# Kernel optimization log

Measured on AMD Instinct MI355X. Metric: run time of the kernel, lower is better.

## Reference

```python
import jax, jax.numpy as jnp
import numpy as np

D_MODEL = 768
D_STATE = 16
D_CONV = 4
EXPAND = 2
INNER = EXPAND * D_MODEL  # 1536
BATCH = 2
SEQLEN = 2048


def setup_inputs() -> dict:
    key = jax.random.key(0)
    ks = jax.random.split(key, 8)
    s = 0.02
    return {
        "hidden_states": jax.random.normal(ks[0], (BATCH, SEQLEN, D_MODEL), jnp.float32),
        "in_proj_w": jax.random.normal(ks[1], (2 * INNER, D_MODEL), jnp.float32) * (D_MODEL ** -0.5),
        "out_proj_w": jax.random.normal(ks[2], (D_MODEL, INNER), jnp.float32) * (INNER ** -0.5),
        "dt_proj_w": jax.random.normal(ks[3], (INNER, INNER), jnp.float32) * (INNER ** -0.5),
        "dt_proj_b": jnp.zeros((INNER,), jnp.float32),
        "conv_w": jax.random.normal(ks[4], (INNER, D_CONV), jnp.float32) * s,
        "conv_b": jnp.zeros((INNER,), jnp.float32),
        "A_log": jnp.zeros((INNER, D_STATE), jnp.float32),
        "B_param": jax.random.normal(ks[5], (INNER, D_STATE), jnp.float32) * s,
        "C_param": jax.random.normal(ks[6], (INNER, D_STATE), jnp.float32) * s,
        "D_param": jnp.ones((INNER,), jnp.float32),
        "dt_bias": jnp.zeros((INNER,), jnp.float32),
    }


def reference(hidden_states, in_proj_w, out_proj_w, dt_proj_w, dt_proj_b,
              conv_w, conv_b, A_log, B_param, C_param, D_param, dt_bias):
    # in_proj: (B, L, d_model) -> (B, L, 2*inner); split into projected / gate
    xz = jnp.einsum('bld,od->blo', hidden_states, in_proj_w)
    proj, gate = jnp.split(xz, 2, axis=-1)
    x = jnp.transpose(proj, (0, 2, 1))  # (B, inner, L) channel-first

    # depthwise causal conv (left-pad d_conv-1) + bias + SiLU
    conv = jax.lax.conv_general_dilated(
        x, conv_w[:, None, :], window_strides=(1,),
        padding=[(D_CONV - 1, 0)], feature_group_count=INNER,
        dimension_numbers=('NCH', 'OIH', 'NCH'))
    u = jax.nn.silu(conv + conv_b[None, :, None])  # (B, inner, L)

    # dt projection (1x1 linear on channel-first) + softplus(dt + dt_bias)
    delta = jnp.einsum('oc,bcl->bol', dt_proj_w, u) + dt_proj_b[None, :, None]
    dt = jax.nn.softplus(delta + dt_bias[None, :, None])  # (B, inner, L)

    A = -jnp.exp(A_log)  # (inner, d_state)
    # discretize: dA = exp(dt * A), dBu = dt * u * B   -> (B, inner, L, N)
    dA = jnp.exp(dt[..., None] * A[None, :, None, :])
    dBu = (dt * u)[..., None] * B_param[None, :, None, :]

    dA_t = jnp.moveaxis(dA, 2, 0)    # (L, B, inner, N)
    dBu_t = jnp.moveaxis(dBu, 2, 0)  # (L, B, inner, N)

    def step(h, inp):
        a_t, b_t = inp
        h = a_t * h + b_t                      # (B, inner, N)
        y = jnp.einsum('bdn,dn->bd', h, C_param)
        return h, y

    h0 = jnp.zeros(dA_t.shape[1:], dA.dtype)
    _, ys = jax.lax.scan(step, h0, (dA_t, dBu_t))  # ys: (L, B, inner)
    y = jnp.transpose(ys, (1, 2, 0))               # (B, inner, L)

    z = jnp.transpose(gate, (0, 2, 1))             # (B, inner, L)
    y = (y + D_param[None, :, None] * u) * jax.nn.silu(z)

    # out_proj: (B, inner, L) -> (B, L, d_model)
    return jnp.einsum('bdl,od->blo', y, out_proj_w)
```

## Files before the change

kernel.cpp:

```cpp
#include <hip/hip_runtime.h>
#include <cstdint>
#include <cstddef>

#define D_MODEL 768
#define D_STATE 16
#define D_CONV  4
#define INNER   1536
#define BATCH   2
#define SEQLEN  2048
#define M_TOK   (BATCH * SEQLEN)
#define NCH     (BATCH * INNER)
#define NCHUNK  64
#define CL      (SEQLEN / NCHUNK)

typedef unsigned short u16;
typedef __attribute__((ext_vector_type(4))) unsigned short us4;
typedef __attribute__((ext_vector_type(8))) short bf8;
typedef __attribute__((ext_vector_type(4))) float f32x4;
typedef __attribute__((ext_vector_type(4))) int i32x4;

#define INV254 (1.f / 254.f)

__device__ __forceinline__ u16 f2bf(float f) {
    uint32_t x = __float_as_uint(f);
    return (u16)((x + 0x7fffu + ((x >> 16) & 1u)) >> 16);
}
__device__ __forceinline__ float bf2f(u16 h) {
    return __uint_as_float(((uint32_t)h) << 16);
}
__device__ __forceinline__ int pk8(float a, float b, float c, float d) {
    return ((int)a & 0xff) | (((int)b & 0xff) << 8) |
           (((int)c & 0xff) << 16) | (((int)d & 0xff) << 24);
}

__global__ __launch_bounds__(256) void rowquant(
    const float* __restrict__ src, int8_t* __restrict__ q1,
    int8_t* __restrict__ q0, float* __restrict__ sc, int K)
{
    const int row = blockIdx.x;
    const float* r = src + (size_t)row * K;
    const int tid = threadIdx.x;

    float mx = 0.f;
    for (int i = tid * 4; i < K; i += 1024) {
        const float4 v = *(const float4*)(r + i);
        mx = fmaxf(mx, fmaxf(fmaxf(fabsf(v.x), fabsf(v.y)),
                             fmaxf(fabsf(v.z), fabsf(v.w))));
    }
#pragma unroll
    for (int off = 1; off < 64; off <<= 1)
        mx = fmaxf(mx, __shfl_xor(mx, off, 64));
    __shared__ float red[4];
    if ((tid & 63) == 0) red[tid >> 6] = mx;
    __syncthreads();
    const float rm = fmaxf(fmaxf(red[0], red[1]), fmaxf(red[2], red[3]));
    const float q = rm > 0.f ? 127.f / rm : 0.f;

    for (int i = tid * 4; i < K; i += 1024) {
        const float4 v = *(const float4*)(r + i);
        float s1[4], s0[4];
        const float xv[4] = {v.x, v.y, v.z, v.w};
#pragma unroll
        for (int e = 0; e < 4; ++e) {
            const float t = xv[e] * q;
            s1[e] = rintf(t);
            s0[e] = rintf((t - s1[e]) * 254.f);
        }
        const size_t o = ((size_t)row * K + i) >> 2;
        ((int*)q1)[o] = pk8(s1[0], s1[1], s1[2], s1[3]);
        ((int*)q0)[o] = pk8(s0[0], s0[1], s0[2], s0[3]);
    }
    if (tid == 0) sc[row] = rm * (1.f / 127.f);
}

__global__ __launch_bounds__(256) void cvt_hilo(
    const float* __restrict__ x, u16* __restrict__ hi, u16* __restrict__ lo, int n4)
{
    const int i = blockIdx.x * 256 + threadIdx.x;
    if (i >= n4) return;
    const float4 v = ((const float4*)x)[i];
    us4 h, l;
    h.x = f2bf(v.x); l.x = f2bf(v.x - bf2f(h.x));
    h.y = f2bf(v.y); l.y = f2bf(v.y - bf2f(h.y));
    h.z = f2bf(v.z); l.z = f2bf(v.z - bf2f(h.z));
    h.w = f2bf(v.w); l.w = f2bf(v.w - bf2f(h.w));
    ((us4*)hi)[i] = h;
    ((us4*)lo)[i] = l;
}

template <int MODE, int FRM, int FRN>
__global__ __launch_bounds__(256) void gemm_i8(
    const int8_t* __restrict__ A1g, const int8_t* __restrict__ A0g,
    const int8_t* __restrict__ B1g, const int8_t* __restrict__ B0g,
    const float* __restrict__ scA, const float* __restrict__ scB,
    float* __restrict__ C, const float* __restrict__ bias1,
    const float* __restrict__ bias2, int M, int N, int K)
{
    constexpr int BM = FRM * 32;
    constexpr int BN = FRN * 32;
    constexpr int SBUF = (BM + BN) * 128;
    __shared__ __align__(16) char smem[2 * SBUF];

    const int tid = threadIdx.x;
    const int w = tid >> 6;
    const int lane = tid & 63;

    const int gx = gridDim.x;
    const int nwg = gx * gridDim.y;
    int f = blockIdx.y * gx + blockIdx.x;
    f = (f & 7) * (nwg >> 3) + (f >> 3);
    const int bm = (f / gx) * BM;
    const int bn = (f % gx) * BN;

    const int wm = (w >> 1) * (FRM * 16);
    const int wn = (w & 1) * (FRN * 16);

    const int g8 = lane & 7;
    const int r8 = lane >> 3;
    const int srcg = g8 ^ r8;
    const int sbyte = (srcg & 3) * 16;
    const bool use_lo = (srcg & 4) != 0;

    const int8_t* pA[FRM];
    const int8_t* pB[FRN];
#pragma unroll
    for (int c = 0; c < FRM; ++c) {
        const int row = w * (FRM * 8) + c * 8 + r8;
        pA[c] = (use_lo ? A0g : A1g) + (size_t)(bm + row) * K + sbyte;
    }
#pragma unroll
    for (int c = 0; c < FRN; ++c) {
        const int row = w * (FRN * 8) + c * 8 + r8;
        pB[c] = (use_lo ? B0g : B1g) + (size_t)(bn + row) * K + sbyte;
    }

    i32x4 acc1[FRM][FRN] = {};
    i32x4 acc2[FRM][FRN] = {};
    const int fr = lane & 15;
    const int gk = lane >> 4;
    const int ghi = gk ^ (fr & 7);

    const int aoff1 = (wm + fr) * 128 + ghi * 16;
    const int aoff0 = (wm + fr) * 128 + (ghi ^ 4) * 16;
    const int boff1 = BM * 128 + (wn + fr) * 128 + ghi * 16;
    const int boff0 = BM * 128 + (wn + fr) * 128 + (ghi ^ 4) * 16;
    const char* const S0 = smem;
    const char* const S1 = smem + SBUF;

    const int nt = K >> 6;

#define STAGE_ALL(sb, kt)                                                           \
    {                                                                               \
        _Pragma("unroll")                                                           \
        for (int c = 0; c < FRM; ++c)                                               \
            __builtin_amdgcn_global_load_lds(                                       \
                (const __attribute__((address_space(1))) void*)(pA[c] + (kt)),      \
                (__attribute__((address_space(3))) void*)((char*)(sb) + (w * FRM + c) * 1024), \
                16, 0, 0);                                                          \
        _Pragma("unroll")                                                           \
        for (int c = 0; c < FRN; ++c)                                               \
            __builtin_amdgcn_global_load_lds(                                       \
                (const __attribute__((address_space(1))) void*)(pB[c] + (kt)),      \
                (__attribute__((address_space(3))) void*)((char*)(sb) + BM * 128 + (w * FRN + c) * 1024), \
                16, 0, 0);                                                          \
    }

#define WAIT_COUNTED()                                                              \
    if constexpr (FRM + FRN == 8) { asm volatile("s_waitcnt vmcnt(8)" ::: "memory"); } \
    else if constexpr (FRM + FRN == 6) { asm volatile("s_waitcnt vmcnt(6)" ::: "memory"); } \
    else { asm volatile("s_waitcnt vmcnt(4)" ::: "memory"); }

#define COMPUTE(S)                                                                  \
    {                                                                               \
        i32x4 a1[FRM], a0[FRM], b1[FRN], b0[FRN];                                   \
        _Pragma("unroll")                                                           \
        for (int i = 0; i < FRM; ++i) {                                             \
            a1[i] = *(const i32x4*)((S) + aoff1 + i * 2048);                        \
            a0[i] = *(const i32x4*)((S) + aoff0 + i * 2048);                        \
        }                                                                           \
        _Pragma("unroll")                                                           \
        for (int j = 0; j < FRN; ++j) {                                             \
            b1[j] = *(const i32x4*)((S) + boff1 + j * 2048);                        \
            b0[j] = *(const i32x4*)((S) + boff0 + j * 2048);                        \
        }                                                                           \
        _Pragma("unroll")                                                           \
        for (int i = 0; i < FRM; ++i)                                               \
            _Pragma("unroll")                                                       \
            for (int j = 0; j < FRN; ++j) {                                         \
                acc1[i][j] = __builtin_amdgcn_mfma_i32_16x16x64_i8(a1[i], b1[j], acc1[i][j], 0, 0, 0); \
                acc2[i][j] = __builtin_amdgcn_mfma_i32_16x16x64_i8(a1[i], b0[j], acc2[i][j], 0, 0, 0); \
                acc2[i][j] = __builtin_amdgcn_mfma_i32_16x16x64_i8(a0[i], b1[j], acc2[i][j], 0, 0, 0); \
            }                                                                       \
    }

    STAGE_ALL(S0, 0)

    for (int t = 0; t < nt; t += 2) {
        STAGE_ALL(S1, (t + 1) * 64)
        WAIT_COUNTED()
        __builtin_amdgcn_s_barrier();
        __builtin_amdgcn_sched_barrier(0);
        __builtin_amdgcn_s_setprio(1);
        COMPUTE(S0)
        __builtin_amdgcn_s_setprio(0);
        __builtin_amdgcn_sched_barrier(0);
        __builtin_amdgcn_s_barrier();

        const int k2 = (t + 2 < nt) ? (t + 2) * 64 : (nt - 1) * 64;
        STAGE_ALL(S0, k2)
        WAIT_COUNTED()
        __builtin_amdgcn_s_barrier();
        __builtin_amdgcn_sched_barrier(0);
        __builtin_amdgcn_s_setprio(1);
        COMPUTE(S1)
        __builtin_amdgcn_s_setprio(0);
        __builtin_amdgcn_sched_barrier(0);
        __builtin_amdgcn_s_barrier();
    }
#undef STAGE_ALL
#undef WAIT_COUNTED
#undef COMPUTE

    const int r0 = (lane >> 4) * 4;
#pragma unroll
    for (int i = 0; i < FRM; ++i) {
        const int row0 = bm + wm + i * 16 + r0;
        float sA[4];
#pragma unroll
        for (int r = 0; r < 4; ++r) sA[r] = scA[row0 + r];
#pragma unroll
        for (int j = 0; j < FRN; ++j) {
            const int col = bn + wn + j * 16 + fr;
            const float sB = scB[col];
            float add = 0.f;
            if constexpr (MODE == 1) add = bias1[col] + bias2[col];
#pragma unroll
            for (int r = 0; r < 4; ++r) {
                float v = ((float)acc1[i][j][r] +
                           (float)acc2[i][j][r] * INV254) * (sA[r] * sB);
                if constexpr (MODE == 1) {
                    const float xx = v + add;
                    v = (xx > 20.f) ? xx : log1pf(expf(xx));
                }
                C[(size_t)(row0 + r) * N + col] = v;
            }
        }
    }
}

template <int MODE, int FRM, int FRN>
__global__ __launch_bounds__(256) void gemm_mfma(
    const u16* __restrict__ Ah_g, const u16* __restrict__ Al_g,
    const u16* __restrict__ Bh_g, const u16* __restrict__ Bl_g,
    float* __restrict__ C, const float* __restrict__ bias1,
    const float* __restrict__ bias2, int M, int N, int K)
{
    constexpr int BM = FRM * 32;
    constexpr int BN = FRN * 32;
    constexpr int SBUF = (BM + BN) * 128;
    __shared__ __align__(16) char smem[2 * SBUF];

    const int tid = threadIdx.x;
    const int w = tid >> 6;
    const int lane = tid & 63;

    const int gx = gridDim.x;
    const int nwg = gx * gridDim.y;
    int f = blockIdx.y * gx + blockIdx.x;
    f = (f & 7) * (nwg >> 3) + (f >> 3);
    const int bm = (f / gx) * BM;
    const int bn = (f % gx) * BN;

    const int wm = (w >> 1) * (FRM * 16);
    const int wn = (w & 1) * (FRN * 16);

    const int g8 = lane & 7;
    const int r8 = lane >> 3;
    const int srcg = g8 ^ r8;
    const int scol = (srcg & 3) * 8;
    const bool use_lo = (srcg & 4) != 0;

    const u16* pA[FRM];
    const u16* pB[FRN];
#pragma unroll
    for (int c = 0; c < FRM; ++c) {
        const int row = w * (FRM * 8) + c * 8 + r8;
        pA[c] = (use_lo ? Al_g : Ah_g) + (size_t)(bm + row) * K + scol;
    }
#pragma unroll
    for (int c = 0; c < FRN; ++c) {
        const int row = w * (FRN * 8) + c * 8 + r8;
        pB[c] = (use_lo ? Bl_g : Bh_g) + (size_t)(bn + row) * K + scol;
    }

    f32x4 acc[FRM][FRN] = {};
    const int fr = lane & 15;
    const int gk = lane >> 4;
    const int ghi = gk ^ (fr & 7);

    const int aoff_h = (wm + fr) * 128 + ghi * 16;
    const int aoff_l = (wm + fr) * 128 + (ghi ^ 4) * 16;
    const int boff_h = BM * 128 + (wn + fr) * 128 + ghi * 16;
    const int boff_l = BM * 128 + (wn + fr) * 128 + (ghi ^ 4) * 16;
    const char* const S0 = smem;
    const char* const S1 = smem + SBUF;

    const int nt = K >> 5;

#define STAGE_ALL(sb, kt)                                                           \
    {                                                                               \
        _Pragma("unroll")                                                           \
        for (int c = 0; c < FRM; ++c)                                               \
            __builtin_amdgcn_global_load_lds(                                       \
                (const __attribute__((address_space(1))) void*)(pA[c] + (kt)),      \
                (__attribute__((address_space(3))) void*)((char*)(sb) + (w * FRM + c) * 1024), \
                16, 0, 0);                                                          \
        _Pragma("unroll")                                                           \
        for (int c = 0; c < FRN; ++c)                                               \
            __builtin_amdgcn_global_load_lds(                                       \
                (const __attribute__((address_space(1))) void*)(pB[c] + (kt)),      \
                (__attribute__((address_space(3))) void*)((char*)(sb) + BM * 128 + (w * FRN + c) * 1024), \
                16, 0, 0);                                                          \
    }

#define WAIT_COUNTED()                                                              \
    if constexpr (FRM + FRN == 8) { asm volatile("s_waitcnt vmcnt(8)" ::: "memory"); } \
    else if constexpr (FRM + FRN == 6) { asm volatile("s_waitcnt vmcnt(6)" ::: "memory"); } \
    else { asm volatile("s_waitcnt vmcnt(4)" ::: "memory"); }

#define COMPUTE(S)                                                                  \
    {                                                                               \
        bf8 ah[FRM], al[FRM], bh[FRN], bl[FRN];                                     \
        _Pragma("unroll")                                                           \
        for (int i = 0; i < FRM; ++i) {                                             \
            ah[i] = *(const bf8*)((S) + aoff_h + i * 2048);                         \
            al[i] = *(const bf8*)((S) + aoff_l + i * 2048);                         \
        }                                                                           \
        _Pragma("unroll")                                                           \
        for (int j = 0; j < FRN; ++j) {                                             \
            bh[j] = *(const bf8*)((S) + boff_h + j * 2048);                         \
            bl[j] = *(const bf8*)((S) + boff_l + j * 2048);                         \
        }                                                                           \
        _Pragma("unroll")                                                           \
        for (int i = 0; i < FRM; ++i)                                               \
            _Pragma("unroll")                                                       \
            for (int j = 0; j < FRN; ++j) {                                         \
                acc[i][j] = __builtin_amdgcn_mfma_f32_16x16x32_bf16(ah[i], bh[j], acc[i][j], 0, 0, 0); \
                acc[i][j] = __builtin_amdgcn_mfma_f32_16x16x32_bf16(ah[i], bl[j], acc[i][j], 0, 0, 0); \
                acc[i][j] = __builtin_amdgcn_mfma_f32_16x16x32_bf16(al[i], bh[j], acc[i][j], 0, 0, 0); \
            }                                                                       \
    }

    STAGE_ALL(S0, 0)

    for (int t = 0; t < nt; t += 2) {
        STAGE_ALL(S1, (t + 1) * 32)
        WAIT_COUNTED()
        __builtin_amdgcn_s_barrier();
        __builtin_amdgcn_sched_barrier(0);
        __builtin_amdgcn_s_setprio(1);
        COMPUTE(S0)
        __builtin_amdgcn_s_setprio(0);
        __builtin_amdgcn_sched_barrier(0);
        __builtin_amdgcn_s_barrier();

        const int k2 = (t + 2 < nt) ? (t + 2) * 32 : (nt - 1) * 32;
        STAGE_ALL(S0, k2)
        WAIT_COUNTED()
        __builtin_amdgcn_s_barrier();
        __builtin_amdgcn_sched_barrier(0);
        __builtin_amdgcn_s_setprio(1);
        COMPUTE(S1)
        __builtin_amdgcn_s_setprio(0);
        __builtin_amdgcn_sched_barrier(0);
        __builtin_amdgcn_s_barrier();
    }
#undef STAGE_ALL
#undef WAIT_COUNTED
#undef COMPUTE

    const int r0 = (lane >> 4) * 4;
#pragma unroll
    for (int i = 0; i < FRM; ++i) {
        const int row0 = bm + wm + i * 16 + r0;
#pragma unroll
        for (int j = 0; j < FRN; ++j) {
            const int col = bn + wn + j * 16 + fr;
            float add = 0.f;
            if constexpr (MODE == 1) add = bias1[col] + bias2[col];
#pragma unroll
            for (int r = 0; r < 4; ++r) {
                float v = acc[i][j][r];
                if constexpr (MODE == 1) {
                    const float xx = v + add;
                    v = (xx > 20.f) ? xx : log1pf(expf(xx));
                }
                C[(size_t)(row0 + r) * N + col] = v;
            }
        }
    }
}

__global__ __launch_bounds__(384) void conv_silu_quant(
    const float* __restrict__ xz, const float* __restrict__ cw,
    const float* __restrict__ cb, int8_t* __restrict__ u1,
    int8_t* __restrict__ u0, float* __restrict__ su)
{
    const int m = blockIdx.x;
    const int tid = threadIdx.x;
    const int c4 = tid * 4;
    const int b = m >> 11;
    const int l = m & (SEQLEN - 1);

    float wt[4][4];
#pragma unroll
    for (int i = 0; i < 4; ++i) {
        const float4 wv = *(const float4*)&cw[(c4 + i) * 4];
        wt[i][0] = wv.x; wt[i][1] = wv.y; wt[i][2] = wv.z; wt[i][3] = wv.w;
    }
    const float4 bias = *(const float4*)&cb[c4];
    float a[4] = {bias.x, bias.y, bias.z, bias.w};

#pragma unroll
    for (int j = 0; j < 4; ++j) {
        const int ll = l - 3 + j;
        if (ll >= 0) {
            const float4 x = *(const float4*)&xz[(size_t)(b * SEQLEN + ll) * (2 * INNER) + c4];
            a[0] = fmaf(x.x, wt[0][j], a[0]);
            a[1] = fmaf(x.y, wt[1][j], a[1]);
            a[2] = fmaf(x.z, wt[2][j], a[2]);
            a[3] = fmaf(x.w, wt[3][j], a[3]);
        }
    }
    float o[4];
#pragma unroll
    for (int i = 0; i < 4; ++i) o[i] = a[i] / (1.f + __expf(-a[i]));

    float mx = fmaxf(fmaxf(fabsf(o[0]), fabsf(o[1])),
                     fmaxf(fabsf(o[2]), fabsf(o[3])));
#pragma unroll
    for (int off = 1; off < 64; off <<= 1)
        mx = fmaxf(mx, __shfl_xor(mx, off, 64));
    __shared__ float red[6];
    if ((tid & 63) == 0) red[tid >> 6] = mx;
    __syncthreads();
    float rm = red[0];
#pragma unroll
    for (int i = 1; i < 6; ++i) rm = fmaxf(rm, red[i]);
    const float q = rm > 0.f ? 127.f / rm : 0.f;

    float s1[4], s0[4];
#pragma unroll
    for (int e = 0; e < 4; ++e) {
        const float t = o[e] * q;
        s1[e] = rintf(t);
        s0[e] = rintf((t - s1[e]) * 254.f);
    }
    const size_t vi = ((size_t)m * INNER + c4) >> 2;
    ((int*)u1)[vi] = pk8(s1[0], s1[1], s1[2], s1[3]);
    ((int*)u0)[vi] = pk8(s0[0], s0[1], s0[2], s0[3]);
    if (tid == 0) su[m] = rm * (1.f / 127.f);
}

__global__ __launch_bounds__(256) void scan_pass1(
    const float* __restrict__ dt, const int8_t* __restrict__ u1,
    const int8_t* __restrict__ u0, const float* __restrict__ su,
    const float* __restrict__ A_log, const float* __restrict__ Bp,
    float* __restrict__ hend, float* __restrict__ Sdt)
{
    const int ch = blockIdx.x * 256 + threadIdx.x;
    const int c = blockIdx.y;
    const int b = (ch >= INNER) ? 1 : 0;
    const int d = ch - b * INNER;

    float A2[D_STATE], Bn[D_STATE];
#pragma unroll
    for (int n = 0; n < D_STATE; n += 4) {
        const float4 av = *(const float4*)&A_log[d * D_STATE + n];
        const float4 bv = *(const float4*)&Bp[d * D_STATE + n];
        A2[n+0] = -expf(av.x) * 1.44269504f; Bn[n+0] = bv.x;
        A2[n+1] = -expf(av.y) * 1.44269504f; Bn[n+1] = bv.y;
        A2[n+2] = -expf(av.z) * 1.44269504f; Bn[n+2] = bv.z;
        A2[n+3] = -expf(av.w) * 1.44269504f; Bn[n+3] = bv.w;
    }

    const size_t base = (size_t)(b * SEQLEN + c * CL) * INNER + d;
    const float* dtp = dt + base;
    const int8_t* u1p = u1 + base;
    const int8_t* u0p = u0 + base;
    const float* sup = su + (b * SEQLEN + c * CL);

    float h[D_STATE] = {};
    float S = 0.f;

    float dtv = dtp[0];
    float uv = fmaf((float)u0p[0], INV254, (float)u1p[0]) * sup[0];

    for (int l = 0; l < CL; ++l) {
        float dtn = 0.f, un = 0.f;
        if (l + 1 < CL) {
            dtn = dtp[(size_t)(l + 1) * INNER];
            un = fmaf((float)u0p[(size_t)(l + 1) * INNER], INV254,
                      (float)u1p[(size_t)(l + 1) * INNER]) * sup[l + 1];
        }
        const float dtu = dtv * uv;
        S += dtv;
#pragma unroll
        for (int n = 0; n < D_STATE; ++n) {
            const float dA = exp2f(dtv * A2[n]);
            h[n] = fmaf(dA, h[n], dtu * Bn[n]);
        }
        dtv = dtn; uv = un;
    }

#pragma unroll
    for (int n = 0; n < D_STATE; ++n)
        hend[((size_t)c * D_STATE + n) * NCH + ch] = h[n];
    Sdt[(size_t)c * NCH + ch] = S;
}

__global__ __launch_bounds__(256) void scan_combine(
    const float* __restrict__ hend, const float* __restrict__ Sdt,
    const float* __restrict__ A_log, float* __restrict__ h0all)
{
    const int idx = blockIdx.x * 256 + threadIdx.x;
    const int n = idx / NCH;
    const int ch = idx - n * NCH;
    const int b = (ch >= INNER) ? 1 : 0;
    const int d = ch - b * INNER;
    const float A2 = -expf(A_log[d * D_STATE + n]) * 1.44269504f;

    float h0 = 0.f;
    for (int c = 0; c < NCHUNK; ++c) {
        const size_t o = ((size_t)c * D_STATE + n) * NCH + ch;
        h0all[o] = h0;
        const float P = exp2f(A2 * Sdt[(size_t)c * NCH + ch]);
        h0 = fmaf(P, h0, hend[o]);
    }
}

__global__ __launch_bounds__(256) void scan_pass2(
    const float* __restrict__ dt, const int8_t* __restrict__ u1,
    const int8_t* __restrict__ u0, const float* __restrict__ su,
    const float* __restrict__ xz, const float* __restrict__ A_log,
    const float* __restrict__ Bp, const float* __restrict__ Cp,
    const float* __restrict__ Dp, const float* __restrict__ h0all,
    u16* __restrict__ ygh, u16* __restrict__ ygl)
{
    const int ch = blockIdx.x * 256 + threadIdx.x;
    const int c = blockIdx.y;
    const int b = (ch >= INNER) ? 1 : 0;
    const int d = ch - b * INNER;

    float A2[D_STATE], Bn[D_STATE], Cn[D_STATE];
#pragma unroll
    for (int n = 0; n < D_STATE; n += 4) {
        const float4 av = *(const float4*)&A_log[d * D_STATE + n];
        const float4 bv = *(const float4*)&Bp[d * D_STATE + n];
        const float4 cv = *(const float4*)&Cp[d * D_STATE + n];
        A2[n+0] = -expf(av.x) * 1.44269504f; Bn[n+0] = bv.x; Cn[n+0] = cv.x;
        A2[n+1] = -expf(av.y) * 1.44269504f; Bn[n+1] = bv.y; Cn[n+1] = cv.y;
        A2[n+2] = -expf(av.z) * 1.44269504f; Bn[n+2] = bv.z; Cn[n+2] = cv.z;
        A2[n+3] = -expf(av.w) * 1.44269504f; Bn[n+3] = bv.w; Cn[n+3] = cv.w;
    }
    const float Dd = Dp[d];

    float h[D_STATE];
#pragma unroll
    for (int n = 0; n < D_STATE; ++n)
        h[n] = h0all[((size_t)c * D_STATE + n) * NCH + ch];

    const size_t base = (size_t)(b * SEQLEN + c * CL) * INNER + d;
    const float* dtp = dt + base;
    const int8_t* u1p = u1 + base;
    const int8_t* u0p = u0 + base;
    const float* sup = su + (b * SEQLEN + c * CL);
    const float* zp = xz + (size_t)(b * SEQLEN + c * CL) * (2 * INNER) + INNER + d;
    u16* yhp = ygh + base;
    u16* ylp = ygl + base;

    float dtv = dtp[0];
    float uv = fmaf((float)u0p[0], INV254, (float)u1p[0]) * sup[0];
    float zv = zp[0];

    for (int l = 0; l < CL; ++l) {
        float dtn = 0.f, un = 0.f, zn = 0.f;
        if (l + 1 < CL) {
            dtn = dtp[(size_t)(l + 1) * INNER];
            un = fmaf((float)u0p[(size_t)(l + 1) * INNER], INV254,
                      (float)u1p[(size_t)(l + 1) * INNER]) * sup[l + 1];
            zn = zp[(size_t)(l + 1) * (2 * INNER)];
        }
        const float dtu = dtv * uv;
        float y = 0.f;
#pragma unroll
        for (int n = 0; n < D_STATE; ++n) {
            const float dA = exp2f(dtv * A2[n]);
            h[n] = fmaf(dA, h[n], dtu * Bn[n]);
            y = fmaf(h[n], Cn[n], y);
        }
        const float sig = 1.f / (1.f + __expf(-zv));
        const float val = (y + Dd * uv) * (zv * sig);
        const u16 hv = f2bf(val);
        yhp[(size_t)l * INNER] = hv;
        ylp[(size_t)l * INNER] = f2bf(val - bf2f(hv));
        dtv = dtn; uv = un; zv = zn;
    }
}

extern "C" void kernel_launch(void* const* d_in, const int* in_sizes, int n_in,
                              void* d_out, int out_size, void* d_ws, size_t ws_size,
                              hipStream_t stream)
{
    const float* hs      = (const float*)d_in[0];
    const float* in_w    = (const float*)d_in[1];
    const float* out_w   = (const float*)d_in[2];
    const float* dt_w    = (const float*)d_in[3];
    const float* dt_b    = (const float*)d_in[4];
    const float* conv_w  = (const float*)d_in[5];
    const float* conv_b  = (const float*)d_in[6];
    const float* A_log   = (const float*)d_in[7];
    const float* Bp      = (const float*)d_in[8];
    const float* Cp      = (const float*)d_in[9];
    const float* Dp      = (const float*)d_in[10];
    const float* dt_bias = (const float*)d_in[11];
    float* out = (float*)d_out;

    float* xz    = (float*)d_ws;
    float* dtf   = xz + (size_t)M_TOK * 2 * INNER;
    float* hend  = dtf + (size_t)M_TOK * INNER;
    float* Sdt   = hend + (size_t)NCHUNK * D_STATE * NCH;
    float* h0all = Sdt + (size_t)NCHUNK * NCH;
    float* su_u  = h0all + (size_t)NCHUNK * D_STATE * NCH;
    float* sc_hs = su_u + M_TOK;
    float* sc_iw = sc_hs + M_TOK;
    float* sc_dw = sc_iw + 2 * INNER;
    u16* ygh = (u16*)(sc_dw + INNER);
    u16* ygl = ygh + (size_t)M_TOK * INNER;
    u16* owh = ygl + (size_t)M_TOK * INNER;
    u16* owl = owh + (size_t)D_MODEL * INNER;
    int8_t* hs1 = (int8_t*)(owl + (size_t)D_MODEL * INNER);
    int8_t* hs0 = hs1 + (size_t)M_TOK * D_MODEL;
    int8_t* iw1 = hs0 + (size_t)M_TOK * D_MODEL;
    int8_t* iw0 = iw1 + (size_t)2 * INNER * D_MODEL;
    int8_t* dw1 = iw0 + (size_t)2 * INNER * D_MODEL;
    int8_t* dw0 = dw1 + (size_t)INNER * INNER;
    int8_t* u1  = dw0 + (size_t)INNER * INNER;
    int8_t* u0  = u1 + (size_t)M_TOK * INNER;

    const dim3 blk(256);

    rowquant<<<dim3(M_TOK), blk, 0, stream>>>(hs, hs1, hs0, sc_hs, D_MODEL);
    rowquant<<<dim3(2 * INNER), blk, 0, stream>>>(in_w, iw1, iw0, sc_iw, D_MODEL);
    rowquant<<<dim3(INNER), blk, 0, stream>>>(dt_w, dw1, dw0, sc_dw, INNER);
    cvt_hilo<<<dim3((D_MODEL * INNER / 4 + 255) / 256), blk, 0, stream>>>(
        out_w, owh, owl, D_MODEL * INNER / 4);

    gemm_i8<0, 4, 4><<<dim3(2 * INNER / 128, M_TOK / 128), blk, 0, stream>>>(
        hs1, hs0, iw1, iw0, sc_hs, sc_iw, xz, nullptr, nullptr,
        M_TOK, 2 * INNER, D_MODEL);

    conv_silu_quant<<<dim3(M_TOK), dim3(384), 0, stream>>>(
        xz, conv_w, conv_b, u1, u0, su_u);

    gemm_i8<1, 4, 2><<<dim3(INNER / 64, M_TOK / 128), blk, 0, stream>>>(
        u1, u0, dw1, dw0, su_u, sc_dw, dtf, dt_b, dt_bias,
        M_TOK, INNER, INNER);

    scan_pass1<<<dim3(NCH / 256, NCHUNK), blk, 0, stream>>>(
        dtf, u1, u0, su_u, A_log, Bp, hend, Sdt);
    scan_combine<<<dim3((D_STATE * NCH) / 256), blk, 0, stream>>>(
        hend, Sdt, A_log, h0all);
    scan_pass2<<<dim3(NCH / 256, NCHUNK), blk, 0, stream>>>(
        dtf, u1, u0, su_u, xz, A_log, Bp, Cp, Dp, h0all, ygh, ygl);

    gemm_mfma<0, 2, 2><<<dim3(D_MODEL / 64, M_TOK / 64), blk, 0, stream>>>(
        ygh, ygl, owh, owl, out, nullptr, nullptr, M_TOK, D_MODEL, INNER);
}
```

Before: 303.6 us.

## Merge prep kernels, store dt in bf16, double scan chunk count

```diff
diff --git a/kernel.cpp b/kernel.cpp
--- a/kernel.cpp
+++ b/kernel.cpp
@@ -10,7 +10,7 @@
 #define SEQLEN  2048
 #define M_TOK   (BATCH * SEQLEN)
 #define NCH     (BATCH * INNER)
-#define NCHUNK  64
+#define NCHUNK  128
 #define CL      (SEQLEN / NCHUNK)
 
 typedef unsigned short u16;
@@ -33,14 +33,40 @@
            (((int)c & 0xff) << 16) | (((int)d & 0xff) << 24);
 }
 
-__global__ __launch_bounds__(256) void rowquant(
-    const float* __restrict__ src, int8_t* __restrict__ q1,
-    int8_t* __restrict__ q0, float* __restrict__ sc, int K)
-{
-    const int row = blockIdx.x;
+__global__ __launch_bounds__(256) void prep_all(
+    const float* __restrict__ hs, int8_t* __restrict__ hs1, int8_t* __restrict__ hs0, float* __restrict__ sc_hs,
+    const float* __restrict__ iw, int8_t* __restrict__ iw1, int8_t* __restrict__ iw0, float* __restrict__ sc_iw,
+    const float* __restrict__ dw, int8_t* __restrict__ dw1, int8_t* __restrict__ dw0, float* __restrict__ sc_dw,
+    const float* __restrict__ ow, u16* __restrict__ owh, u16* __restrict__ owl)
+{
+    const int blk = blockIdx.x;
+    const int tid = threadIdx.x;
+
+    if (blk >= M_TOK + 2 * INNER + INNER) {
+        const int j = (blk - (M_TOK + 3 * INNER)) * 256 + tid;
+        const int n4 = D_MODEL * INNER / 4;
+        if (j >= n4) return;
+        const float4 v = ((const float4*)ow)[j];
+        us4 h, l;
+        h.x = f2bf(v.x); l.x = f2bf(v.x - bf2f(h.x));
+        h.y = f2bf(v.y); l.y = f2bf(v.y - bf2f(h.y));
+        h.z = f2bf(v.z); l.z = f2bf(v.z - bf2f(h.z));
+        h.w = f2bf(v.w); l.w = f2bf(v.w - bf2f(h.w));
+        ((us4*)owh)[j] = h;
+        ((us4*)owl)[j] = l;
+        return;
+    }
+
+    const float* src; int8_t* q1; int8_t* q0; float* sc; int K; int row;
+    if (blk < M_TOK) {
+        src = hs; q1 = hs1; q0 = hs0; sc = sc_hs; K = D_MODEL; row = blk;
+    } else if (blk < M_TOK + 2 * INNER) {
+        src = iw; q1 = iw1; q0 = iw0; sc = sc_iw; K = D_MODEL; row = blk - M_TOK;
+    } else {
+        src = dw; q1 = dw1; q0 = dw0; sc = sc_dw; K = INNER; row = blk - M_TOK - 2 * INNER;
+    }
+
     const float* r = src + (size_t)row * K;
-    const int tid = threadIdx.x;
-
     float mx = 0.f;
     for (int i = tid * 4; i < K; i += 1024) {
         const float4 v = *(const float4*)(r + i);
@@ -73,27 +99,12 @@
     if (tid == 0) sc[row] = rm * (1.f / 127.f);
 }
 
-__global__ __launch_bounds__(256) void cvt_hilo(
-    const float* __restrict__ x, u16* __restrict__ hi, u16* __restrict__ lo, int n4)
-{
-    const int i = blockIdx.x * 256 + threadIdx.x;
-    if (i >= n4) return;
-    const float4 v = ((const float4*)x)[i];
-    us4 h, l;
-    h.x = f2bf(v.x); l.x = f2bf(v.x - bf2f(h.x));
-    h.y = f2bf(v.y); l.y = f2bf(v.y - bf2f(h.y));
-    h.z = f2bf(v.z); l.z = f2bf(v.z - bf2f(h.z));
-    h.w = f2bf(v.w); l.w = f2bf(v.w - bf2f(h.w));
-    ((us4*)hi)[i] = h;
-    ((us4*)lo)[i] = l;
-}
-
 template <int MODE, int FRM, int FRN>
 __global__ __launch_bounds__(256) void gemm_i8(
     const int8_t* __restrict__ A1g, const int8_t* __restrict__ A0g,
     const int8_t* __restrict__ B1g, const int8_t* __restrict__ B0g,
     const float* __restrict__ scA, const float* __restrict__ scB,
-    float* __restrict__ C, const float* __restrict__ bias1,
+    void* __restrict__ Cv, const float* __restrict__ bias1,
     const float* __restrict__ bias2, int M, int N, int K)
 {
     constexpr int BM = FRM * 32;
@@ -241,8 +252,10 @@
                 if constexpr (MODE == 1) {
                     const float xx = v + add;
                     v = (xx > 20.f) ? xx : log1pf(expf(xx));
+                    ((u16*)Cv)[(size_t)(row0 + r) * N + col] = f2bf(v);
+                } else {
+                    ((float*)Cv)[(size_t)(row0 + r) * N + col] = v;
                 }
-                C[(size_t)(row0 + r) * N + col] = v;
             }
         }
     }
@@ -463,7 +476,7 @@
 }
 
 __global__ __launch_bounds__(256) void scan_pass1(
-    const float* __restrict__ dt, const int8_t* __restrict__ u1,
+    const u16* __restrict__ dtb, const int8_t* __restrict__ u1,
     const int8_t* __restrict__ u0, const float* __restrict__ su,
     const float* __restrict__ A_log, const float* __restrict__ Bp,
     float* __restrict__ hend, float* __restrict__ Sdt)
@@ -485,7 +498,7 @@
     }
 
     const size_t base = (size_t)(b * SEQLEN + c * CL) * INNER + d;
-    const float* dtp = dt + base;
+    const u16* dtp = dtb + base;
     const int8_t* u1p = u1 + base;
     const int8_t* u0p = u0 + base;
     const float* sup = su + (b * SEQLEN + c * CL);
@@ -493,13 +506,13 @@
     float h[D_STATE] = {};
     float S = 0.f;
 
-    float dtv = dtp[0];
+    float dtv = bf2f(dtp[0]);
     float uv = fmaf((float)u0p[0], INV254, (float)u1p[0]) * sup[0];
 
     for (int l = 0; l < CL; ++l) {
         float dtn = 0.f, un = 0.f;
         if (l + 1 < CL) {
-            dtn = dtp[(size_t)(l + 1) * INNER];
+            dtn = bf2f(dtp[(size_t)(l + 1) * INNER]);
             un = fmaf((float)u0p[(size_t)(l + 1) * INNER], INV254,
                       (float)u1p[(size_t)(l + 1) * INNER]) * sup[l + 1];
         }
@@ -540,7 +553,7 @@
 }
 
 __global__ __launch_bounds__(256) void scan_pass2(
-    const float* __restrict__ dt, const int8_t* __restrict__ u1,
+    const u16* __restrict__ dtb, const int8_t* __restrict__ u1,
     const int8_t* __restrict__ u0, const float* __restrict__ su,
     const float* __restrict__ xz, const float* __restrict__ A_log,
     const float* __restrict__ Bp, const float* __restrict__ Cp,
@@ -571,7 +584,7 @@
         h[n] = h0all[((size_t)c * D_STATE + n) * NCH + ch];
 
     const size_t base = (size_t)(b * SEQLEN + c * CL) * INNER + d;
-    const float* dtp = dt + base;
+    const u16* dtp = dtb + base;
     const int8_t* u1p = u1 + base;
     const int8_t* u0p = u0 + base;
     const float* sup = su + (b * SEQLEN + c * CL);
@@ -579,14 +592,14 @@
     u16* yhp = ygh + base;
     u16* ylp = ygl + base;
 
-    float dtv = dtp[0];
+    float dtv = bf2f(dtp[0]);
     float uv = fmaf((float)u0p[0], INV254, (float)u1p[0]) * sup[0];
     float zv = zp[0];
 
     for (int l = 0; l < CL; ++l) {
         float dtn = 0.f, un = 0.f, zn = 0.f;
         if (l + 1 < CL) {
-            dtn = dtp[(size_t)(l + 1) * INNER];
+            dtn = bf2f(dtp[(size_t)(l + 1) * INNER]);
             un = fmaf((float)u0p[(size_t)(l + 1) * INNER], INV254,
                       (float)u1p[(size_t)(l + 1) * INNER]) * sup[l + 1];
             zn = zp[(size_t)(l + 1) * (2 * INNER)];
@@ -627,15 +640,15 @@
     float* out = (float*)d_out;
 
     float* xz    = (float*)d_ws;
-    float* dtf   = xz + (size_t)M_TOK * 2 * INNER;
-    float* hend  = dtf + (size_t)M_TOK * INNER;
+    float* hend  = xz + (size_t)M_TOK * 2 * INNER;
     float* Sdt   = hend + (size_t)NCHUNK * D_STATE * NCH;
     float* h0all = Sdt + (size_t)NCHUNK * NCH;
     float* su_u  = h0all + (size_t)NCHUNK * D_STATE * NCH;
     float* sc_hs = su_u + M_TOK;
     float* sc_iw = sc_hs + M_TOK;
     float* sc_dw = sc_iw + 2 * INNER;
-    u16* ygh = (u16*)(sc_dw + INNER);
+    u16* dtb = (u16*)(sc_dw + INNER);
+    u16* ygh = dtb + (size_t)M_TOK * INNER;
     u16* ygl = ygh + (size_t)M_TOK * INNER;
     u16* owh = ygl + (size_t)M_TOK * INNER;
     u16* owl = owh + (size_t)D_MODEL * INNER;
@@ -650,11 +663,13 @@
 
     const dim3 blk(256);
 
-    rowquant<<<dim3(M_TOK), blk, 0, stream>>>(hs, hs1, hs0, sc_hs, D_MODEL);
-    rowquant<<<dim3(2 * INNER), blk, 0, stream>>>(in_w, iw1, iw0, sc_iw, D_MODEL);
-    rowquant<<<dim3(INNER), blk, 0, stream>>>(dt_w, dw1, dw0, sc_dw, INNER);
-    cvt_hilo<<<dim3((D_MODEL * INNER / 4 + 255) / 256), blk, 0, stream>>>(
-        out_w, owh, owl, D_MODEL * INNER / 4);
+    {
+        const int nq = M_TOK + 2 * INNER + INNER;
+        const int nc = (D_MODEL * INNER / 4 + 255) / 256;
+        prep_all<<<dim3(nq + nc), blk, 0, stream>>>(
+            hs, hs1, hs0, sc_hs, in_w, iw1, iw0, sc_iw,
+            dt_w, dw1, dw0, sc_dw, out_w, owh, owl);
+    }
 
     gemm_i8<0, 4, 4><<<dim3(2 * INNER / 128, M_TOK / 128), blk, 0, stream>>>(
         hs1, hs0, iw1, iw0, sc_hs, sc_iw, xz, nullptr, nullptr,
@@ -664,15 +679,15 @@
         xz, conv_w, conv_b, u1, u0, su_u);
 
     gemm_i8<1, 4, 2><<<dim3(INNER / 64, M_TOK / 128), blk, 0, stream>>>(
-        u1, u0, dw1, dw0, su_u, sc_dw, dtf, dt_b, dt_bias,
+        u1, u0, dw1, dw0, su_u, sc_dw, dtb, dt_b, dt_bias,
         M_TOK, INNER, INNER);
 
     scan_pass1<<<dim3(NCH / 256, NCHUNK), blk, 0, stream>>>(
-        dtf, u1, u0, su_u, A_log, Bp, hend, Sdt);
+        dtb, u1, u0, su_u, A_log, Bp, hend, Sdt);
     scan_combine<<<dim3((D_STATE * NCH) / 256), blk, 0, stream>>>(
         hend, Sdt, A_log, h0all);
     scan_pass2<<<dim3(NCH / 256, NCHUNK), blk, 0, stream>>>(
-        dtf, u1, u0, su_u, xz, A_log, Bp, Cp, Dp, h0all, ygh, ygl);
+        dtb, u1, u0, su_u, xz, A_log, Bp, Cp, Dp, h0all, ygh, ygl);
 
     gemm_mfma<0, 2, 2><<<dim3(D_MODEL / 64, M_TOK / 64), blk, 0, stream>>>(
         ygh, ygl, owh, owl, out, nullptr, nullptr, M_TOK, D_MODEL, INNER);
```

After: 306.0 us. Within noise of the previous version (+0.8%).
